# Kernel tuning notes

Measured on AMD Instinct MI355X. Metric: run time of the kernel, lower is better.

## Reference

```python
import jax, jax.numpy as jnp
import numpy as np

B, N, C_Q, H, C_HID = 1, 2048, 256, 8, 32


def setup_inputs() -> dict:
    key = jax.random.key(0)
    ks = jax.random.split(key, 8)
    s_in = 1.0 / np.sqrt(C_Q)
    s_hid = 1.0 / np.sqrt(H * C_HID)
    return {
        "q_x": jax.random.normal(ks[0], (B, N, C_Q), jnp.float32),
        "kv_x": jax.random.normal(ks[1], (B, N, C_Q), jnp.float32),
        "attn_bias": jax.random.normal(ks[2], (B, H, N, N), jnp.float32),
        "Wq": jax.random.normal(ks[3], (C_Q, H * C_HID), jnp.float32) * s_in,
        "Wk": jax.random.normal(ks[4], (C_Q, H * C_HID), jnp.float32) * s_in,
        "Wv": jax.random.normal(ks[5], (C_Q, H * C_HID), jnp.float32) * s_in,
        "Wg": jax.random.normal(ks[6], (C_Q, H * C_HID), jnp.float32) * s_in,
        "Wo": jax.random.normal(ks[7], (H * C_HID, C_Q), jnp.float32) * s_hid,
    }


def reference(q_x, kv_x, attn_bias, Wq, Wk, Wv, Wg, Wo):
    # QKV projections (no bias), split heads: [B, H, N, C_hid]
    def proj(x, W):
        y = x @ W  # [B, N, H*C_hid]
        return y.reshape(y.shape[:-1] + (H, C_HID)).swapaxes(-2, -3)

    scale = 1.0 / np.sqrt(C_HID)
    q = proj(q_x, Wq) * scale
    k = proj(kv_x, Wk)
    v = proj(kv_x, Wv)

    # scores + external additive bias, stable softmax
    scores = jnp.einsum("bhqc,bhkc->bhqk", q, k) + attn_bias
    a = jax.nn.softmax(scores, axis=-1)
    o = jnp.einsum("bhqk,bhkc->bhqc", a, v)  # [B, H, N, C_hid]

    o = o.swapaxes(-2, -3)  # [B, N, H, C_hid]
    # sigmoid gating from query input
    g = jax.nn.sigmoid(q_x @ Wg).reshape(o.shape)
    o = o * g
    o = o.reshape(o.shape[:-2] + (H * C_HID,))
    return o @ Wo  # [B, N, C_q]
```

## Files before the change

### kernel.cpp

```cpp
#include <hip/hip_runtime.h>
#include <hip/hip_bf16.h>
#include <stdint.h>

typedef __attribute__((ext_vector_type(8))) short short8;
typedef __attribute__((ext_vector_type(8))) __bf16 bf16x8;
typedef __attribute__((ext_vector_type(4))) float f32x4;
typedef __attribute__((ext_vector_type(4))) float float4v;
typedef __attribute__((ext_vector_type(4))) unsigned short us4;
typedef unsigned int u32;
typedef __attribute__((ext_vector_type(2))) u32 u32x2;
typedef __attribute__((address_space(3))) u32 lds_u32;
typedef const __attribute__((address_space(1))) u32 g_u32;

#define NSEQ 2048
#define L2E 1.44269504088896f
#define SMAX 16.0f

static __device__ __forceinline__ unsigned short f2bf(float x){
  union { float f; u32 u; } v; v.f = x;
  u32 r = v.u + 0x7fffu + ((v.u >> 16) & 1u);
  return (unsigned short)(r >> 16);
}
static __device__ __forceinline__ float bf2f(unsigned short s){
  union { float f; u32 u; } v; v.u = ((u32)s) << 16; return v.f;
}
static __device__ __forceinline__ u32 cvtpk(float lo, float hi){
  u32 r; asm("v_cvt_pk_bf16_f32 %0, %1, %2" : "=v"(r) : "v"(lo), "v"(hi)); return r;
}
static __device__ __forceinline__ void gload16(const void* g, void* l){
  __builtin_amdgcn_global_load_lds((g_u32*)g, (lds_u32*)l, 16, 0, 0);
}
static __device__ __forceinline__ f32x4 mfma16(bf16x8 a, bf16x8 b, f32x4 c){
  return __builtin_amdgcn_mfma_f32_16x16x32_bf16(a, b, c, 0, 0, 0);
}
static __device__ __forceinline__ bf16x8 ldfrag(const void* p){
  return *(const bf16x8*)p;
}
#define MEMFENCE() asm volatile("" ::: "memory")

__global__ __launch_bounds__(256) void cvt_kernel(const float* __restrict__ qx,
                           const float* __restrict__ kvx,
                           const float* __restrict__ Wq, const float* __restrict__ Wk,
                           const float* __restrict__ Wv, const float* __restrict__ Wg,
                           const float* __restrict__ Wo,
                           unsigned short* __restrict__ Xbq, unsigned short* __restrict__ Xbkv,
                           unsigned short* __restrict__ Wt4, unsigned short* __restrict__ Wot){
  __shared__ float T[64][65];
  int bid = blockIdx.x;
  if (bid < 512){
    int i4 = (bid*256 + threadIdx.x) * 4;
    float4v q = *(const float4v*)(qx + i4);
    float4v k = *(const float4v*)(kvx + i4);
    us4 qo, ko;
    #pragma unroll
    for (int j = 0; j < 4; ++j){ qo[j] = f2bf(q[j]); ko[j] = f2bf(k[j]); }
    *(us4*)(Xbq + i4) = qo;
    *(us4*)(Xbkv + i4) = ko;
  } else {
    int b2 = bid - 512;
    int w = b2 >> 4, tile = b2 & 15, tr = tile >> 2, tc = tile & 3;
    const float* W = (w==0)?Wq:((w==1)?Wk:((w==2)?Wv:((w==3)?Wg:Wo)));
    int t = threadIdx.x;
    int rl = t >> 4, cq = t & 15;
    #pragma unroll
    for (int p = 0; p < 4; ++p){
      int r = p*16 + rl;
      float4v v = *(const float4v*)(W + (size_t)(tr*64 + r)*256 + tc*64 + cq*4);
      #pragma unroll
      for (int j = 0; j < 4; ++j) T[r][cq*4+j] = v[j];
    }
    __syncthreads();
    float s = (w==0) ? 0.17677669529663687f : 1.f;
    #pragma unroll
    for (int p = 0; p < 4; ++p){
      int o = p*16 + rl;
      us4 pk;
      #pragma unroll
      for (int j = 0; j < 4; ++j) pk[j] = f2bf(T[cq*4+j][o] * s);
      int og = tc*64 + o, ig = tr*64 + cq*4;
      if (w < 4) *(us4*)(Wt4 + (size_t)w*65536 + og*256 + ig) = pk;
      else       *(us4*)(Wot + (size_t)og*256 + ig) = pk;
    }
  }
}

__global__ __launch_bounds__(256) void proj_kernel(const unsigned short* __restrict__ Xbq,
     const unsigned short* __restrict__ Xbkv, const unsigned short* __restrict__ Wt4,
     unsigned short* __restrict__ Qb, unsigned short* __restrict__ Kb,
     unsigned short* __restrict__ Vt, unsigned short* __restrict__ Gg){
  __shared__ unsigned short Asm[64*256];
  __shared__ unsigned short Bsm[64*256];
  int mt = blockIdx.x;
  int nt = blockIdx.y;
  int col0 = nt * 64;
  int w = col0 >> 8;
  const unsigned short* A = (w==0 || w==3) ? Xbq : Xbkv;
  int tid = threadIdx.x, lane = tid & 63, wid = tid >> 6;
  const char* Ab = (const char*)A   + (size_t)mt*64*512;
  const char* Bb = (const char*)Wt4 + (size_t)col0*512;
  char* Asl = (char*)Asm; char* Bsl = (char*)Bsm;
  #pragma unroll
  for (int it = 0; it < 8; ++it){
    int o = it*4096 + wid*1024 + lane*16;
    int row = o >> 9, b = o & 511;
    int sb = (o & ~511) + (b ^ ((row & 15) << 4));
    gload16(Ab + sb, Asl + it*4096 + wid*1024);
    gload16(Bb + sb, Bsl + it*4096 + wid*1024);
  }
  __syncthreads();
  int ml = lane & 15, kg = lane >> 4;
  int m = wid*16 + ml;
  bf16x8 afr[8];
  #pragma unroll
  for (int ks = 0; ks < 8; ++ks)
    afr[ks] = ldfrag(Asl + m*512 + ((ks*64 + kg*16) ^ (ml << 4)));
  f32x4 acc[4];
  #pragma unroll
  for (int ct = 0; ct < 4; ++ct){
    acc[ct] = (f32x4){0.f,0.f,0.f,0.f};
    int oo = ct*16 + ml;
    #pragma unroll
    for (int ks = 0; ks < 8; ++ks){
      bf16x8 bfr = ldfrag(Bsl + oo*512 + ((ks*64 + kg*16) ^ (ml << 4)));
      acc[ct] = mfma16(afr[ks], bfr, acc[ct]);
    }
  }
  #pragma unroll
  for (int ct = 0; ct < 4; ++ct){
    int colg = col0 + ct*16 + ml;
    int cw = colg & 255, hh = cw >> 5, c = cw & 31;
    int n0 = mt*64 + wid*16 + kg*4;
    if (w == 2){
      us4 pk;
      pk[0]=f2bf(acc[ct][0]); pk[1]=f2bf(acc[ct][1]);
      pk[2]=f2bf(acc[ct][2]); pk[3]=f2bf(acc[ct][3]);
      *(us4*)((char*)Vt + ((size_t)(hh*32 + c)*NSEQ + n0)*2) = pk;
    } else {
      #pragma unroll
      for (int r = 0; r < 4; ++r){
        int n = n0 + r;
        float v = acc[ct][r];
        if (w == 0)      Qb[((size_t)hh*NSEQ + n)*32 + c] = f2bf(v);
        else if (w == 1) Kb[((size_t)hh*NSEQ + n)*32 + c] = f2bf(v);
        else             Gg[(size_t)n*256 + cw] = f2bf(1.f/(1.f + __expf(-v)));
      }
    }
  }
}

__global__ __launch_bounds__(256) void attn_kernel(const unsigned short* __restrict__ Qb,
    const unsigned short* __restrict__ Kb, const unsigned short* __restrict__ Vt,
    const float* __restrict__ bias,
    float* __restrict__ Opart, float* __restrict__ Lpart){
  __shared__ unsigned short Ksm[4][2048];
  __shared__ unsigned short Vsm[4][2048];
  __shared__ unsigned short Psm[4096];
  int bid = blockIdx.x;
  int h = bid >> 7, qt = (bid >> 2) & 31, ch = bid & 3;
  int q0 = qt * 64;
  int tid = threadIdx.x, lane = tid & 63, wid = tid >> 6;
  int ml = lane & 15, kg = lane >> 4;
  int qw = q0 + wid*16;
  bf16x8 qfr = ldfrag((const char*)Qb + (((size_t)h*NSEQ + qw + ml)*32 + kg*8)*2);
  const char* Kbase = (const char*)Kb + (size_t)h*NSEQ*32*2;
  const char* Vbase = (const char*)Vt + (size_t)h*32*NSEQ*2;
  const float* bias_q = bias + (size_t)h*NSEQ*NSEQ + (size_t)(qw + ml)*NSEQ + ch*512 + kg*4;
  float lreg = 0.f;
  f32x4 oacc[2];
  oacc[0] = (f32x4){0.f,0.f,0.f,0.f};
  oacc[1] = (f32x4){0.f,0.f,0.f,0.f};

  auto stage = [&](int t, int buf){
    int tg = ch*8 + t;
    int o = tid*16;
    int n = o >> 6, kb = o & 63;
    gload16(Kbase + (size_t)tg*4096 + (o & ~63) + (kb ^ (((n>>1)&3) << 4)),
            (char*)&Ksm[buf][0] + o);
    int c = o >> 7, vb = o & 127;
    gload16(Vbase + (size_t)c*4096 + (size_t)tg*128 + (vb ^ ((c&7) << 4)),
            (char*)&Vsm[buf][0] + o);
  };

  float4v bb[4];
  #pragma unroll
  for (int ct = 0; ct < 4; ++ct) bb[ct] = *(const float4v*)(bias_q + ct*16);
  MEMFENCE();
  stage(0, 0);
  stage(1, 1);
  int qrow = wid*16 + ml;
  char* Pb = (char*)Psm + qrow*128;
  int qs = (ml & 7) << 4;
  for (int t = 0; t < 8; ++t){
    int cur = t & 3;
    if (t == 7) asm volatile("s_waitcnt vmcnt(0)" ::: "memory");
    else        asm volatile("s_waitcnt vmcnt(2)" ::: "memory");
    __builtin_amdgcn_s_barrier();
    MEMFENCE();
    f32x4 s[4];
    #pragma unroll
    for (int ct = 0; ct < 4; ++ct){
      int n = ct*16 + ml;
      bf16x8 kfr = ldfrag((char*)&Ksm[cur][0] + n*64 + ((kg*16) ^ (((n>>1)&3) << 4)));
      f32x4 b;
      #pragma unroll
      for (int r = 0; r < 4; ++r) b[r] = bb[ct][r];
      s[ct] = mfma16(kfr, qfr, b);
    }
    MEMFENCE();
    if (t < 7){
      #pragma unroll
      for (int ct = 0; ct < 4; ++ct)
        bb[ct] = *(const float4v*)(bias_q + (t+1)*64 + ct*16);
    }
    MEMFENCE();
    if (t < 6) stage(t+2, (t+2) & 3);
    MEMFENCE();
    float rs = 0.f;
    #pragma unroll
    for (int ct = 0; ct < 4; ++ct){
      #pragma unroll
      for (int r = 0; r < 4; ++r){
        float pv = exp2f((s[ct][r] - SMAX) * L2E);
        s[ct][r] = pv;
        rs += pv;
      }
    }
    rs += __shfl_xor(rs, 16);
    rs += __shfl_xor(rs, 32);
    lreg += rs;
    #pragma unroll
    for (int ct = 0; ct < 4; ++ct){
      u32x2 pk;
      pk[0] = cvtpk(s[ct][0], s[ct][1]);
      pk[1] = cvtpk(s[ct][2], s[ct][3]);
      *(u32x2*)(Pb + ((ct*32 + kg*8) ^ qs)) = pk;
    }
    #pragma unroll
    for (int ks = 0; ks < 2; ++ks){
      bf16x8 pfr = ldfrag(Pb + ((ks*64 + kg*16) ^ qs));
      #pragma unroll
      for (int c2 = 0; c2 < 2; ++c2){
        int c = c2*16 + ml;
        bf16x8 vfr = ldfrag((char*)&Vsm[cur][0] + c*128 + ((ks*64 + kg*16) ^ ((c&7) << 4)));
        oacc[c2] = mfma16(pfr, vfr, oacc[c2]);
      }
    }
    MEMFENCE();
  }
  size_t pbase = ((size_t)(ch*8 + h)*NSEQ);
  if (kg == 0){
    Lpart[pbase + qw + ml] = lreg;
  }
  #pragma unroll
  for (int c2 = 0; c2 < 2; ++c2){
    #pragma unroll
    for (int r = 0; r < 4; ++r){
      int q = qw + kg*4 + r;
      Opart[(pbase + q)*32 + c2*16 + ml] = oacc[c2][r];
    }
  }
}

__global__ __launch_bounds__(256) void combine_kernel(const float* __restrict__ Opart,
    const float* __restrict__ Lpart,
    const unsigned short* __restrict__ Gg, unsigned short* __restrict__ Og){
  int n = blockIdx.x*8 + (threadIdx.x >> 5);
  int c = threadIdx.x & 31;
  #pragma unroll
  for (int h = 0; h < 8; ++h){
    float L = Lpart[(size_t)(0*8+h)*NSEQ + n] + Lpart[(size_t)(1*8+h)*NSEQ + n]
            + Lpart[(size_t)(2*8+h)*NSEQ + n] + Lpart[(size_t)(3*8+h)*NSEQ + n];
    float o = Opart[((size_t)(0*8+h)*NSEQ + n)*32 + c]
            + Opart[((size_t)(1*8+h)*NSEQ + n)*32 + c]
            + Opart[((size_t)(2*8+h)*NSEQ + n)*32 + c]
            + Opart[((size_t)(3*8+h)*NSEQ + n)*32 + c];
    float g = bf2f(Gg[(size_t)n*256 + h*32 + c]);
    Og[(size_t)n*256 + h*32 + c] = f2bf(o / L * g);
  }
}

__global__ __launch_bounds__(256) void oproj_kernel(const unsigned short* __restrict__ Og,
    const unsigned short* __restrict__ Wot, float* __restrict__ out){
  __shared__ unsigned short Asm[64*256];
  __shared__ unsigned short Bsm[64*256];
  int mt = blockIdx.x, nt = blockIdx.y;
  int col0 = nt * 64;
  int tid = threadIdx.x, lane = tid & 63, wid = tid >> 6;
  const char* Ab = (const char*)Og  + (size_t)mt*64*512;
  const char* Bb = (const char*)Wot + (size_t)col0*512;
  char* Asl = (char*)Asm; char* Bsl = (char*)Bsm;
  #pragma unroll
  for (int it = 0; it < 8; ++it){
    int o = it*4096 + wid*1024 + lane*16;
    int row = o >> 9, b = o & 511;
    int sb = (o & ~511) + (b ^ ((row & 15) << 4));
    gload16(Ab + sb, Asl + it*4096 + wid*1024);
    gload16(Bb + sb, Bsl + it*4096 + wid*1024);
  }
  __syncthreads();
  int ml = lane & 15, kg = lane >> 4;
  int m = wid*16 + ml;
  bf16x8 afr[8];
  #pragma unroll
  for (int ks = 0; ks < 8; ++ks)
    afr[ks] = ldfrag(Asl + m*512 + ((ks*64 + kg*16) ^ (ml << 4)));
  f32x4 acc[4];
  #pragma unroll
  for (int ct = 0; ct < 4; ++ct){
    acc[ct] = (f32x4){0.f,0.f,0.f,0.f};
    int oo = ct*16 + ml;
    #pragma unroll
    for (int ks = 0; ks < 8; ++ks){
      bf16x8 bfr = ldfrag(Bsl + oo*512 + ((ks*64 + kg*16) ^ (ml << 4)));
      acc[ct] = mfma16(afr[ks], bfr, acc[ct]);
    }
  }
  #pragma unroll
  for (int ct = 0; ct < 4; ++ct){
    #pragma unroll
    for (int r = 0; r < 4; ++r){
      int mm = mt*64 + wid*16 + kg*4 + r;
      out[(size_t)mm*256 + col0 + ct*16 + ml] = acc[ct][r];
    }
  }
}

extern "C" void kernel_launch(void* const* d_in, const int* in_sizes, int n_in,
                              void* d_out, int out_size, void* d_ws, size_t ws_size,
                              hipStream_t stream) {
  const float* qx   = (const float*)d_in[0];
  const float* kvx  = (const float*)d_in[1];
  const float* bias = (const float*)d_in[2];
  const float* Wq   = (const float*)d_in[3];
  const float* Wk   = (const float*)d_in[4];
  const float* Wv   = (const float*)d_in[5];
  const float* Wg   = (const float*)d_in[6];
  const float* Wo   = (const float*)d_in[7];
  float* out = (float*)d_out;
  char* ws = (char*)d_ws;
  unsigned short* Xbq  = (unsigned short*)(ws);
  unsigned short* Xbkv = (unsigned short*)(ws + (1<<20));
  unsigned short* Wt4  = (unsigned short*)(ws + (2<<20));
  unsigned short* Wot  = (unsigned short*)(ws + (2<<20) + (512<<10));
  unsigned short* Qb   = (unsigned short*)(ws + (3<<20));
  unsigned short* Kb   = (unsigned short*)(ws + (4<<20));
  unsigned short* Vt   = (unsigned short*)(ws + (5<<20));
  unsigned short* Gg   = (unsigned short*)(ws + (6<<20));
  unsigned short* Og   = (unsigned short*)(ws + (7<<20));
  float*          Opart= (float*)(ws + (8<<20));
  float*          Lpart= (float*)(ws + (17<<20));

  cvt_kernel<<<592, 256, 0, stream>>>(qx, kvx, Wq, Wk, Wv, Wg, Wo, Xbq, Xbkv, Wt4, Wot);
  dim3 gp(32, 16);
  proj_kernel<<<gp, 256, 0, stream>>>(Xbq, Xbkv, Wt4, Qb, Kb, Vt, Gg);
  attn_kernel<<<1024, 256, 0, stream>>>(Qb, Kb, Vt, bias, Opart, Lpart);
  combine_kernel<<<256, 256, 0, stream>>>(Opart, Lpart, Gg, Og);
  dim3 go(32, 4);
  oproj_kernel<<<go, 256, 0, stream>>>(Og, Wot, out);
}
```

Before: 51.35 us.

## Fuse combine and output projection into attention via last-block atomic counter

Removes the separate combine and output-projection kernels. Each attention block bumps a per-query-tile atomic counter, and the last of the 32 blocks for that tile (8 heads × 4 key chunks) reduces the partial outputs, applies normalisation and gating, stages the bf16 tile in LDS, and runs the 64×256 output projection reading Wo straight from global memory. This saves two launches and the Og round trip through memory. In exchange, the epilogue runs serialised on a few tail blocks, and it relies on threadfence ordering plus a counter reset inside cvt_kernel.

```diff
diff --git a/kernel.cpp b/kernel.cpp
--- a/kernel.cpp
+++ b/kernel.cpp
@@ -44,9 +44,11 @@
                            const float* __restrict__ Wv, const float* __restrict__ Wg,
                            const float* __restrict__ Wo,
                            unsigned short* __restrict__ Xbq, unsigned short* __restrict__ Xbkv,
-                           unsigned short* __restrict__ Wt4, unsigned short* __restrict__ Wot){
+                           unsigned short* __restrict__ Wt4, unsigned short* __restrict__ Wot,
+                           int* __restrict__ Cnt){
   __shared__ float T[64][65];
   int bid = blockIdx.x;
+  if (bid == 0 && threadIdx.x < 32) Cnt[threadIdx.x] = 0;
   if (bid < 512){
     int i4 = (bid*256 + threadIdx.x) * 4;
     float4v q = *(const float4v*)(qx + i4);
@@ -150,11 +152,14 @@
 
 __global__ __launch_bounds__(256) void attn_kernel(const unsigned short* __restrict__ Qb,
     const unsigned short* __restrict__ Kb, const unsigned short* __restrict__ Vt,
-    const float* __restrict__ bias,
-    float* __restrict__ Opart, float* __restrict__ Lpart){
-  __shared__ unsigned short Ksm[4][2048];
-  __shared__ unsigned short Vsm[4][2048];
-  __shared__ unsigned short Psm[4096];
+    const float* __restrict__ bias, const unsigned short* __restrict__ Gg,
+    const unsigned short* __restrict__ Wot,
+    float* __restrict__ Opart, float* __restrict__ Lpart,
+    int* __restrict__ Cnt, float* __restrict__ out){
+  __shared__ __attribute__((aligned(16))) char LDSBUF[40960];
+  unsigned short (*Ksm)[2048] = (unsigned short(*)[2048])(LDSBUF);
+  unsigned short (*Vsm)[2048] = (unsigned short(*)[2048])(LDSBUF + 16384);
+  unsigned short* Psm = (unsigned short*)(LDSBUF + 32768);
   int bid = blockIdx.x;
   int h = bid >> 7, qt = (bid >> 2) & 31, ch = bid & 3;
   int q0 = qt * 64;
@@ -259,68 +264,74 @@
       Opart[(pbase + q)*32 + c2*16 + ml] = oacc[c2][r];
     }
   }
-}
-
-__global__ __launch_bounds__(256) void combine_kernel(const float* __restrict__ Opart,
-    const float* __restrict__ Lpart,
-    const unsigned short* __restrict__ Gg, unsigned short* __restrict__ Og){
-  int n = blockIdx.x*8 + (threadIdx.x >> 5);
-  int c = threadIdx.x & 31;
-  #pragma unroll
-  for (int h = 0; h < 8; ++h){
-    float L = Lpart[(size_t)(0*8+h)*NSEQ + n] + Lpart[(size_t)(1*8+h)*NSEQ + n]
-            + Lpart[(size_t)(2*8+h)*NSEQ + n] + Lpart[(size_t)(3*8+h)*NSEQ + n];
-    float o = Opart[((size_t)(0*8+h)*NSEQ + n)*32 + c]
-            + Opart[((size_t)(1*8+h)*NSEQ + n)*32 + c]
-            + Opart[((size_t)(2*8+h)*NSEQ + n)*32 + c]
-            + Opart[((size_t)(3*8+h)*NSEQ + n)*32 + c];
-    float g = bf2f(Gg[(size_t)n*256 + h*32 + c]);
-    Og[(size_t)n*256 + h*32 + c] = f2bf(o / L * g);
-  }
-}
-
-__global__ __launch_bounds__(256) void oproj_kernel(const unsigned short* __restrict__ Og,
-    const unsigned short* __restrict__ Wot, float* __restrict__ out){
-  __shared__ unsigned short Asm[64*256];
-  __shared__ unsigned short Bsm[64*256];
-  int mt = blockIdx.x, nt = blockIdx.y;
-  int col0 = nt * 64;
-  int tid = threadIdx.x, lane = tid & 63, wid = tid >> 6;
-  const char* Ab = (const char*)Og  + (size_t)mt*64*512;
-  const char* Bb = (const char*)Wot + (size_t)col0*512;
-  char* Asl = (char*)Asm; char* Bsl = (char*)Bsm;
-  #pragma unroll
-  for (int it = 0; it < 8; ++it){
-    int o = it*4096 + wid*1024 + lane*16;
-    int row = o >> 9, b = o & 511;
-    int sb = (o & ~511) + (b ^ ((row & 15) << 4));
-    gload16(Ab + sb, Asl + it*4096 + wid*1024);
-    gload16(Bb + sb, Bsl + it*4096 + wid*1024);
-  }
+  __threadfence();
   __syncthreads();
-  int ml = lane & 15, kg = lane >> 4;
-  int m = wid*16 + ml;
-  bf16x8 afr[8];
-  #pragma unroll
-  for (int ks = 0; ks < 8; ++ks)
-    afr[ks] = ldfrag(Asl + m*512 + ((ks*64 + kg*16) ^ (ml << 4)));
-  f32x4 acc[4];
-  #pragma unroll
-  for (int ct = 0; ct < 4; ++ct){
-    acc[ct] = (f32x4){0.f,0.f,0.f,0.f};
-    int oo = ct*16 + ml;
-    #pragma unroll
-    for (int ks = 0; ks < 8; ++ks){
-      bf16x8 bfr = ldfrag(Bsl + oo*512 + ((ks*64 + kg*16) ^ (ml << 4)));
-      acc[ct] = mfma16(afr[ks], bfr, acc[ct]);
-    }
-  }
-  #pragma unroll
-  for (int ct = 0; ct < 4; ++ct){
-    #pragma unroll
-    for (int r = 0; r < 4; ++r){
-      int mm = mt*64 + wid*16 + kg*4 + r;
-      out[(size_t)mm*256 + col0 + ct*16 + ml] = acc[ct][r];
+  int* flag = (int*)(LDSBUF + 40952);
+  if (tid == 0) *flag = (atomicAdd(&Cnt[qt], 1) == 31);
+  __syncthreads();
+  if (!*flag) return;
+  __threadfence();
+  {
+    int r = tid >> 2, qd = tid & 3;
+    int n = q0 + r;
+    char* Arow = LDSBUF + r*512;
+    int sw = (r & 15) << 4;
+    #pragma unroll
+    for (int hh2 = 0; hh2 < 2; ++hh2){
+      int hh = qd*2 + hh2;
+      float L = Lpart[(size_t)(0*8+hh)*NSEQ + n] + Lpart[(size_t)(1*8+hh)*NSEQ + n]
+              + Lpart[(size_t)(2*8+hh)*NSEQ + n] + Lpart[(size_t)(3*8+hh)*NSEQ + n];
+      float inv = 1.f / L;
+      const float* P0 = &Opart[((size_t)(0*8+hh)*NSEQ + n)*32];
+      const float* P1 = &Opart[((size_t)(1*8+hh)*NSEQ + n)*32];
+      const float* P2 = &Opart[((size_t)(2*8+hh)*NSEQ + n)*32];
+      const float* P3 = &Opart[((size_t)(3*8+hh)*NSEQ + n)*32];
+      #pragma unroll
+      for (int cq = 0; cq < 8; ++cq){
+        float4v o0 = *(const float4v*)(P0 + cq*4);
+        float4v o1 = *(const float4v*)(P1 + cq*4);
+        float4v o2 = *(const float4v*)(P2 + cq*4);
+        float4v o3 = *(const float4v*)(P3 + cq*4);
+        us4 gg = *(const us4*)(Gg + (size_t)n*256 + hh*32 + cq*4);
+        float v0 = (o0[0] + o1[0] + o2[0] + o3[0]) * inv * bf2f(gg[0]);
+        float v1 = (o0[1] + o1[1] + o2[1] + o3[1]) * inv * bf2f(gg[1]);
+        float v2 = (o0[2] + o1[2] + o2[2] + o3[2]) * inv * bf2f(gg[2]);
+        float v3 = (o0[3] + o1[3] + o2[3] + o3[3]) * inv * bf2f(gg[3]);
+        u32x2 pk;
+        pk[0] = cvtpk(v0, v1);
+        pk[1] = cvtpk(v2, v3);
+        int b = hh*64 + cq*8;
+        *(u32x2*)(Arow + (b ^ sw)) = pk;
+      }
+    }
+  }
+  __syncthreads();
+  {
+    int m = wid*16 + ml;
+    bf16x8 afr[8];
+    #pragma unroll
+    for (int ks = 0; ks < 8; ++ks)
+      afr[ks] = ldfrag(LDSBUF + m*512 + ((ks*64 + kg*16) ^ (ml << 4)));
+    #pragma unroll
+    for (int nt = 0; nt < 4; ++nt){
+      int col0 = nt*64;
+      f32x4 acc[4];
+      #pragma unroll
+      for (int ct = 0; ct < 4; ++ct){
+        acc[ct] = (f32x4){0.f,0.f,0.f,0.f};
+        const char* Brow = (const char*)Wot + (size_t)(col0 + ct*16 + ml)*512 + kg*16;
+        #pragma unroll
+        for (int ks = 0; ks < 8; ++ks)
+          acc[ct] = mfma16(afr[ks], ldfrag(Brow + ks*64), acc[ct]);
+      }
+      #pragma unroll
+      for (int ct = 0; ct < 4; ++ct){
+        #pragma unroll
+        for (int r = 0; r < 4; ++r){
+          int mm = q0 + wid*16 + kg*4 + r;
+          out[(size_t)mm*256 + col0 + ct*16 + ml] = acc[ct][r];
+        }
+      }
     }
   }
 }
@@ -346,15 +357,12 @@
   unsigned short* Kb   = (unsigned short*)(ws + (4<<20));
   unsigned short* Vt   = (unsigned short*)(ws + (5<<20));
   unsigned short* Gg   = (unsigned short*)(ws + (6<<20));
-  unsigned short* Og   = (unsigned short*)(ws + (7<<20));
   float*          Opart= (float*)(ws + (8<<20));
   float*          Lpart= (float*)(ws + (17<<20));
-
-  cvt_kernel<<<592, 256, 0, stream>>>(qx, kvx, Wq, Wk, Wv, Wg, Wo, Xbq, Xbkv, Wt4, Wot);
+  int*            Cnt  = (int*)(ws + (18<<20));
+
+  cvt_kernel<<<592, 256, 0, stream>>>(qx, kvx, Wq, Wk, Wv, Wg, Wo, Xbq, Xbkv, Wt4, Wot, Cnt);
   dim3 gp(32, 16);
   proj_kernel<<<gp, 256, 0, stream>>>(Xbq, Xbkv, Wt4, Qb, Kb, Vt, Gg);
-  attn_kernel<<<1024, 256, 0, stream>>>(Qb, Kb, Vt, bias, Opart, Lpart);
-  combine_kernel<<<256, 256, 0, stream>>>(Opart, Lpart, Gg, Og);
-  dim3 go(32, 4);
-  oproj_kernel<<<go, 256, 0, stream>>>(Og, Wot, out);
-}
+  attn_kernel<<<1024, 256, 0, stream>>>(Qb, Kb, Vt, bias, Gg, Wot, Opart, Lpart, Cnt, out);
+}
```

Result: slower. 195.9 us (+281.5%).

## Process two KV tiles per barrier with double bias prefetch

Applied to the files above, without the earlier changes.

Restructures the attention main loop so each iteration handles two key/value tiles under one barrier, with two bias register sets prefetched one tile pair ahead. All four LDS buffers are filled up front and the softmax/PV step moves into a lambda. The goal is fewer barriers and more independent work between waits. The trade-offs are a full vmcnt(0) wait per pair instead of a partial wait, and the first iteration reloading tiles 2 and 3 that are already resident, which adds redundant global traffic.

```diff
diff --git a/kernel.cpp b/kernel.cpp
--- a/kernel.cpp
+++ b/kernel.cpp
@@ -181,40 +181,11 @@
             (char*)&Vsm[buf][0] + o);
   };
 
-  float4v bb[4];
-  #pragma unroll
-  for (int ct = 0; ct < 4; ++ct) bb[ct] = *(const float4v*)(bias_q + ct*16);
-  MEMFENCE();
-  stage(0, 0);
-  stage(1, 1);
   int qrow = wid*16 + ml;
   char* Pb = (char*)Psm + qrow*128;
   int qs = (ml & 7) << 4;
-  for (int t = 0; t < 8; ++t){
-    int cur = t & 3;
-    if (t == 7) asm volatile("s_waitcnt vmcnt(0)" ::: "memory");
-    else        asm volatile("s_waitcnt vmcnt(2)" ::: "memory");
-    __builtin_amdgcn_s_barrier();
-    MEMFENCE();
-    f32x4 s[4];
-    #pragma unroll
-    for (int ct = 0; ct < 4; ++ct){
-      int n = ct*16 + ml;
-      bf16x8 kfr = ldfrag((char*)&Ksm[cur][0] + n*64 + ((kg*16) ^ (((n>>1)&3) << 4)));
-      f32x4 b;
-      #pragma unroll
-      for (int r = 0; r < 4; ++r) b[r] = bb[ct][r];
-      s[ct] = mfma16(kfr, qfr, b);
-    }
-    MEMFENCE();
-    if (t < 7){
-      #pragma unroll
-      for (int ct = 0; ct < 4; ++ct)
-        bb[ct] = *(const float4v*)(bias_q + (t+1)*64 + ct*16);
-    }
-    MEMFENCE();
-    if (t < 6) stage(t+2, (t+2) & 3);
-    MEMFENCE();
+
+  auto smpv = [&](f32x4* s, int bufV){
     float rs = 0.f;
     #pragma unroll
     for (int ct = 0; ct < 4; ++ct){
@@ -241,10 +212,59 @@
       #pragma unroll
       for (int c2 = 0; c2 < 2; ++c2){
         int c = c2*16 + ml;
-        bf16x8 vfr = ldfrag((char*)&Vsm[cur][0] + c*128 + ((ks*64 + kg*16) ^ ((c&7) << 4)));
+        bf16x8 vfr = ldfrag((char*)&Vsm[bufV][0] + c*128 + ((ks*64 + kg*16) ^ ((c&7) << 4)));
         oacc[c2] = mfma16(pfr, vfr, oacc[c2]);
       }
     }
+  };
+
+  float4v bbA[4], bbB[4];
+  #pragma unroll
+  for (int ct = 0; ct < 4; ++ct) bbA[ct] = *(const float4v*)(bias_q + ct*16);
+  MEMFENCE();
+  #pragma unroll
+  for (int ct = 0; ct < 4; ++ct) bbB[ct] = *(const float4v*)(bias_q + 64 + ct*16);
+  MEMFENCE();
+  stage(0, 0); stage(1, 1); stage(2, 2); stage(3, 3);
+  MEMFENCE();
+
+  for (int p = 0; p < 4; ++p){
+    int bA = (p & 1) << 1, bB = bA | 1;
+    asm volatile("s_waitcnt vmcnt(0)" ::: "memory");
+    __builtin_amdgcn_s_barrier();
+    MEMFENCE();
+    if (p < 3){ stage(2*p+2, bA ^ 2); stage(2*p+3, bB ^ 2); }
+    MEMFENCE();
+    f32x4 s[4];
+    #pragma unroll
+    for (int ct = 0; ct < 4; ++ct){
+      int n = ct*16 + ml;
+      bf16x8 kfr = ldfrag((char*)&Ksm[bA][0] + n*64 + ((kg*16) ^ (((n>>1)&3) << 4)));
+      s[ct] = mfma16(kfr, qfr, bbA[ct]);
+    }
+    MEMFENCE();
+    if (p < 3){
+      #pragma unroll
+      for (int ct = 0; ct < 4; ++ct)
+        bbA[ct] = *(const float4v*)(bias_q + (2*p+2)*64 + ct*16);
+    }
+    MEMFENCE();
+    smpv(s, bA);
+    MEMFENCE();
+    #pragma unroll
+    for (int ct = 0; ct < 4; ++ct){
+      int n = ct*16 + ml;
+      bf16x8 kfr = ldfrag((char*)&Ksm[bB][0] + n*64 + ((kg*16) ^ (((n>>1)&3) << 4)));
+      s[ct] = mfma16(kfr, qfr, bbB[ct]);
+    }
+    MEMFENCE();
+    if (p < 3){
+      #pragma unroll
+      for (int ct = 0; ct < 4; ++ct)
+        bbB[ct] = *(const float4v*)(bias_q + (2*p+3)*64 + ct*16);
+    }
+    MEMFENCE();
+    smpv(s, bB);
     MEMFENCE();
   }
   size_t pbase = ((size_t)(ch*8 + h)*NSEQ);
```

Result: no change. 51.88 us (+1.0%).
